# Kernel optimization log

Measured on AMD Instinct MI355X. Metric: run time of the kernel, lower is better.

The kernel has to match this reference:

```python
import jax, jax.numpy as jnp
import numpy as np

DIM = 1024
NUM_HEADS = 16
HEAD_DIM = DIM // NUM_HEADS
B, N = 4, 2048


def _rope_sin_cos(seq_len, head_dim, dtype=jnp.float32):
    inv_freq = 1.0 / (10000.0 ** (jnp.arange(0, head_dim, 2, dtype=jnp.float32) / head_dim))
    t = jnp.arange(seq_len, dtype=jnp.float32)
    freqs = jnp.einsum('i,j->ij', t, inv_freq)          # [N, head_dim/2]
    emb = jnp.concatenate([freqs, freqs], axis=-1)      # [N, head_dim]
    return jnp.sin(emb).astype(dtype), jnp.cos(emb).astype(dtype)


def _rotate_half(x):
    x1, x2 = jnp.split(x, 2, axis=-1)
    return jnp.concatenate([-x2, x1], axis=-1)


def setup_inputs() -> dict:
    key = jax.random.key(0)
    k1, k2, k3, k4, k5 = jax.random.split(key, 5)
    scale = 0.02
    return {
        'x': jax.random.normal(k1, (B, N, DIM), dtype=jnp.float32),
        'W_qkv': jax.random.normal(k2, (DIM, 3 * DIM), dtype=jnp.float32) * scale,
        'b_qkv': jax.random.normal(k3, (3 * DIM,), dtype=jnp.float32) * scale,
        'W_proj': jax.random.normal(k4, (DIM, DIM), dtype=jnp.float32) * scale,
        'b_proj': jax.random.normal(k5, (DIM,), dtype=jnp.float32) * scale,
    }


def reference(x, W_qkv, b_qkv, W_proj, b_proj):
    Bsz, Nlen, C = x.shape
    H, Dh = NUM_HEADS, HEAD_DIM
    qkv = x @ W_qkv + b_qkv                              # [B, N, 3C]
    q, k, v = jnp.split(qkv, 3, axis=-1)
    # [B, H, N, Dh]
    q = q.reshape(Bsz, Nlen, H, Dh).transpose(0, 2, 1, 3)
    k = k.reshape(Bsz, Nlen, H, Dh).transpose(0, 2, 1, 3)
    v = v.reshape(Bsz, Nlen, H, Dh).transpose(0, 2, 1, 3)
    sin, cos = _rope_sin_cos(Nlen, Dh, x.dtype)          # [N, Dh] each, broadcast
    q = q * cos + _rotate_half(q) * sin
    k = k * cos + _rotate_half(k) * sin
    scale = 1.0 / jnp.sqrt(jnp.asarray(Dh, x.dtype))
    scores = jnp.einsum('bhqd,bhkd->bhqk', q, k) * scale  # [B, H, N, N]
    attn = jax.nn.softmax(scores, axis=-1)
    out = jnp.einsum('bhqk,bhkd->bhqd', attn, v)          # [B, H, N, Dh]
    out = out.transpose(0, 2, 1, 3).reshape(Bsz, Nlen, C)
    return out @ W_proj + b_proj
```

## Files before the change

kernel.cpp:

```cpp
#include <hip/hip_runtime.h>
#include <hip/hip_bf16.h>
#include <math.h>

#define BSZ 4
#define NSEQ 2048
#define CDIM 1024
#define NH 16
#define DH 64
#define KC 64
#define KMAX_STRIDE 32

typedef _Float16 half8_t __attribute__((ext_vector_type(8)));
typedef _Float16 half4_t __attribute__((ext_vector_type(4)));
typedef float floatx4 __attribute__((ext_vector_type(4)));

#define GLOBAL_AS(p) ((const __attribute__((address_space(1))) void*)(p))
#define LDS_AS(p)    ((__attribute__((address_space(3))) void*)(p))

__global__ __launch_bounds__(256) void cast_x_kernel(
    const float* __restrict__ src, _Float16* __restrict__ dst) {
  const size_t i = ((size_t)blockIdx.x * 256 + threadIdx.x) * 8;
  float4 a = *(const float4*)(src + i);
  float4 b = *(const float4*)(src + i + 4);
  half8_t h;
  h[0] = (_Float16)a.x; h[1] = (_Float16)a.y; h[2] = (_Float16)a.z; h[3] = (_Float16)a.w;
  h[4] = (_Float16)b.x; h[5] = (_Float16)b.y; h[6] = (_Float16)b.z; h[7] = (_Float16)b.w;
  *(half8_t*)(dst + i) = h;
}

__global__ __launch_bounds__(256) void transpose_cast_kernel(
    const float* __restrict__ src, _Float16* __restrict__ dst, int R, int C) {
  __shared__ float Ls[64][65];
  const int t = threadIdx.x;
  const int r0 = blockIdx.y * 64, c0 = blockIdx.x * 64;
  {
    const int lr = t >> 2, lcg = (t & 3) * 16;
    const float* s = src + (size_t)(r0 + lr) * C + c0 + lcg;
#pragma unroll
    for (int u = 0; u < 4; ++u)
      *(float4*)&Ls[lr][lcg + 4 * u] = *(const float4*)(s + 4 * u);
  }
  __syncthreads();
  const int c = t >> 2, rg = (t & 3) * 16;
  half8_t h0, h1;
#pragma unroll
  for (int u = 0; u < 8; ++u) h0[u] = (_Float16)Ls[rg + u][c];
#pragma unroll
  for (int u = 0; u < 8; ++u) h1[u] = (_Float16)Ls[rg + 8 + u][c];
  _Float16* d = dst + (size_t)(c0 + c) * R + r0 + rg;
  *(half8_t*)d = h0;
  *(half8_t*)(d + 8) = h1;
}

__global__ __launch_bounds__(256) void qkv_gemm_kernel(
    const _Float16* __restrict__ xh, const _Float16* __restrict__ Wt,
    const float* __restrict__ bias, _Float16* __restrict__ Qh,
    _Float16* __restrict__ Kh, _Float16* __restrict__ Vh) {
  __shared__ _Float16 As[128 * 64];
  __shared__ _Float16 Bs[128 * 64];
  const int tid = threadIdx.x;
  const int lane = tid & 63, w = tid >> 6;
  const int m = lane & 15, quad = lane >> 4;
  const int wr = (w >> 1) * 64, wc = (w & 1) * 64;
  const int m0 = blockIdx.y * 128;
  const int N0 = blockIdx.x * 128;
  const int sr = lane >> 3, sc = (lane & 7) * 8;

  floatx4 acc[4][4];
#pragma unroll
  for (int i = 0; i < 4; ++i)
#pragma unroll
    for (int j = 0; j < 4; ++j) acc[i][j] = (floatx4){0.f, 0.f, 0.f, 0.f};

  for (int k0 = 0; k0 < CDIM; k0 += 64) {
    __syncthreads();
#pragma unroll
    for (int i = 0; i < 4; ++i) {
      const int row = (w * 4 + i) * 8 + sr;
      __builtin_amdgcn_global_load_lds(
          GLOBAL_AS(xh + (size_t)(m0 + row) * CDIM + k0 + sc),
          LDS_AS(As + (w * 4 + i) * 512), 16, 0, 0);
      __builtin_amdgcn_global_load_lds(
          GLOBAL_AS(Wt + (size_t)(N0 + row) * CDIM + k0 + sc),
          LDS_AS(Bs + (w * 4 + i) * 512), 16, 0, 0);
    }
    __syncthreads();
#pragma unroll
    for (int ks = 0; ks < 2; ++ks) {
      half8_t af[4], bf[4];
#pragma unroll
      for (int mt = 0; mt < 4; ++mt)
        af[mt] = *(half8_t*)(As + (wr + mt * 16 + m) * 64 + ks * 32 + quad * 8);
#pragma unroll
      for (int nt = 0; nt < 4; ++nt)
        bf[nt] = *(half8_t*)(Bs + (wc + nt * 16 + m) * 64 + ks * 32 + quad * 8);
#pragma unroll
      for (int mt = 0; mt < 4; ++mt)
#pragma unroll
        for (int nt = 0; nt < 4; ++nt)
          acc[mt][nt] = __builtin_amdgcn_mfma_f32_16x16x32_f16(
              af[mt], bf[nt], acc[mt][nt], 0, 0, 0);
    }
  }

  const int F0 = N0 + wc;
  const int which = F0 >> 10;
  const int head = (F0 & 1023) >> 6;
  float bv[4];
#pragma unroll
  for (int nt = 0; nt < 4; ++nt) bv[nt] = bias[F0 + nt * 16 + m];

  if (which == 2) {
#pragma unroll
    for (int mt = 0; mt < 4; ++mt)
#pragma unroll
      for (int reg = 0; reg < 4; ++reg) {
        const int gm = m0 + wr + mt * 16 + 4 * quad + reg;
        const int b = gm >> 11, n = gm & 2047;
        const size_t vbase = ((size_t)(b * NH + head) * DH) * NSEQ + n;
#pragma unroll
        for (int nt = 0; nt < 4; ++nt)
          Vh[vbase + (size_t)(nt * 16 + m) * NSEQ] =
              (_Float16)(acc[mt][nt][reg] + bv[nt]);
      }
  } else {
    _Float16* dst = which ? Kh : Qh;
    const float qs = which ? 1.0f : 0.125f * 1.4426950408889634f;
    const float invfA = expf(-9.210340371976184f * ((float)m * (1.0f / 32.0f)));
    const float invfB = expf(-9.210340371976184f * ((float)(16 + m) * (1.0f / 32.0f)));
#pragma unroll
    for (int mt = 0; mt < 4; ++mt)
#pragma unroll
      for (int reg = 0; reg < 4; ++reg) {
        const int gm = m0 + wr + mt * 16 + 4 * quad + reg;
        const int b = gm >> 11, n = gm & 2047;
        float sA, cA, sB, cB;
        sincosf((float)n * invfA, &sA, &cA);
        sincosf((float)n * invfB, &sB, &cB);
        const size_t obase = ((size_t)(b * NH + head) * NSEQ + n) * DH;
#pragma unroll
        for (int nt = 0; nt < 4; ++nt) {
          const float val = acc[mt][nt][reg] + bv[nt];
          const float rot = (nt < 2) ? -(acc[mt][nt + 2][reg] + bv[nt + 2])
                                     :  (acc[mt][nt - 2][reg] + bv[nt - 2]);
          const float sv = (nt & 1) ? sB : sA;
          const float cv = (nt & 1) ? cB : cA;
          dst[obase + nt * 16 + m] = (_Float16)((val * cv + rot * sv) * qs);
        }
      }
  }
}

__global__ __launch_bounds__(64) void kmax_init_kernel(unsigned* kmaxu) {
  for (int i = threadIdx.x; i < 64 * KMAX_STRIDE; i += 64) kmaxu[i] = 0u;
}

__global__ __launch_bounds__(256) void qk_norms_kernel(
    const _Float16* __restrict__ Qh, const _Float16* __restrict__ Kh,
    float* __restrict__ qn, unsigned* __restrict__ kmaxu) {
  __shared__ float wmax[4];
  const int tid = threadIdx.x;
  const size_t row = (size_t)blockIdx.x * 32 + (tid >> 3);
  const int c = (tid & 7) * 8;
  half8_t q8 = *(const half8_t*)(Qh + row * DH + c);
  half8_t k8 = *(const half8_t*)(Kh + row * DH + c);
  float qs = 0.f, ks = 0.f;
#pragma unroll
  for (int u = 0; u < 8; ++u) {
    const float qv = (float)q8[u], kv = (float)k8[u];
    qs += qv * qv; ks += kv * kv;
  }
  qs += __shfl_xor(qs, 1, 64); ks += __shfl_xor(ks, 1, 64);
  qs += __shfl_xor(qs, 2, 64); ks += __shfl_xor(ks, 2, 64);
  qs += __shfl_xor(qs, 4, 64); ks += __shfl_xor(ks, 4, 64);
  if ((tid & 7) == 0) qn[row] = sqrtf(qs);
  ks = fmaxf(ks, __shfl_xor(ks, 8, 64));
  ks = fmaxf(ks, __shfl_xor(ks, 16, 64));
  ks = fmaxf(ks, __shfl_xor(ks, 32, 64));
  if ((tid & 63) == 0) wmax[tid >> 6] = ks;
  __syncthreads();
  if (tid == 0) {
    const float mx = fmaxf(fmaxf(wmax[0], wmax[1]), fmaxf(wmax[2], wmax[3]));
    atomicMax(&kmaxu[(row >> 11) * KMAX_STRIDE], __float_as_uint(sqrtf(mx)));
  }
}

__global__ __launch_bounds__(256) void attn_kernel(
    const _Float16* __restrict__ Qh, const _Float16* __restrict__ Kh,
    const _Float16* __restrict__ Vh, const float* __restrict__ qn,
    const unsigned* __restrict__ kmaxu, _Float16* __restrict__ AO) {
  __shared__ char smem[36864];
  _Float16* Ks = (_Float16*)smem;
  _Float16* Vt = (_Float16*)(smem + 9216);
  _Float16* Ps = (_Float16*)(smem + 18432);
  float* Os = (float*)smem;

  const int tid = threadIdx.x;
  const int lane = tid & 63;
  const int w = tid >> 6;
  const int m = lane & 15;
  const int quad = lane >> 4;
  const int bh = blockIdx.y;
  const int q0 = blockIdx.x * 128;

  const _Float16* Qb = Qh + (size_t)bh * NSEQ * DH;
  const _Float16* Kb = Kh + (size_t)bh * NSEQ * DH;
  const _Float16* Vb = Vh + (size_t)bh * DH * NSEQ;

  const int rA = q0 + w * 32 + m;
  const int rB = rA + 16;
  half8_t qfA0 = *(const half8_t*)(Qb + (size_t)rA * DH + quad * 8);
  half8_t qfA1 = *(const half8_t*)(Qb + (size_t)rA * DH + 32 + quad * 8);
  half8_t qfB0 = *(const half8_t*)(Qb + (size_t)rB * DH + quad * 8);
  half8_t qfB1 = *(const half8_t*)(Qb + (size_t)rB * DH + 32 + quad * 8);

  const float kmx = __uint_as_float(kmaxu[bh * KMAX_STRIDE]);
  const float mA = qn[(size_t)bh * NSEQ + rA] * kmx;
  const float mB = qn[(size_t)bh * NSEQ + rB] * kmx;

  float lA = 0.f, lB = 0.f;
  floatx4 OA[4], OB[4];
#pragma unroll
  for (int nb = 0; nb < 4; ++nb) {
    OA[nb] = (floatx4){0.f, 0.f, 0.f, 0.f};
    OB[nb] = (floatx4){0.f, 0.f, 0.f, 0.f};
  }

  _Float16* PwA = Ps + w * 2304 + m * 72;
  _Float16* PwB = PwA + 16 * 72;

  for (int ck = 0; ck < NSEQ / KC; ++ck) {
    const int k0 = ck * KC;
    __syncthreads();
    {
      const _Float16* Kc = Kb + (size_t)k0 * DH;
      const _Float16* Vc = Vb + k0;
      int g = tid;
      int key = g >> 3, dg = g & 7;
      *(half8_t*)(Ks + key * 72 + dg * 8) = *(const half8_t*)(Kc + key * 64 + dg * 8);
      *(half8_t*)(Vt + key * 72 + dg * 8) = *(const half8_t*)(Vc + (size_t)key * NSEQ + dg * 8);
      g = tid + 256;
      key = g >> 3; dg = g & 7;
      *(half8_t*)(Ks + key * 72 + dg * 8) = *(const half8_t*)(Kc + key * 64 + dg * 8);
      *(half8_t*)(Vt + key * 72 + dg * 8) = *(const half8_t*)(Vc + (size_t)key * NSEQ + dg * 8);
    }
    __syncthreads();

    floatx4 stA[4], stB[4];
#pragma unroll
    for (int kt = 0; kt < 4; ++kt) {
      half8_t kf0 = *(half8_t*)(Ks + (kt * 16 + m) * 72 + quad * 8);
      half8_t kf1 = *(half8_t*)(Ks + (kt * 16 + m) * 72 + 32 + quad * 8);
      floatx4 a = (floatx4){0.f, 0.f, 0.f, 0.f};
      a = __builtin_amdgcn_mfma_f32_16x16x32_f16(kf0, qfA0, a, 0, 0, 0);
      a = __builtin_amdgcn_mfma_f32_16x16x32_f16(kf1, qfA1, a, 0, 0, 0);
      stA[kt] = a;
      floatx4 b = (floatx4){0.f, 0.f, 0.f, 0.f};
      b = __builtin_amdgcn_mfma_f32_16x16x32_f16(kf0, qfB0, b, 0, 0, 0);
      b = __builtin_amdgcn_mfma_f32_16x16x32_f16(kf1, qfB1, b, 0, 0, 0);
      stB[kt] = b;
    }

#pragma unroll
    for (int kt = 0; kt < 4; ++kt) {
      half4_t phA, phB;
#pragma unroll
      for (int r = 0; r < 4; ++r) {
        const float pA = __builtin_exp2f(stA[kt][r] - mA);
        const float pB = __builtin_exp2f(stB[kt][r] - mB);
        lA += pA; lB += pB;
        phA[r] = (_Float16)pA; phB[r] = (_Float16)pB;
      }
      *(half4_t*)(PwA + kt * 16 + quad * 4) = phA;
      *(half4_t*)(PwB + kt * 16 + quad * 4) = phB;
    }

#pragma unroll
    for (int c = 0; c < 2; ++c) {
      half8_t pfA = *(half8_t*)(PwA + c * 32 + quad * 8);
      half8_t pfB = *(half8_t*)(PwB + c * 32 + quad * 8);
#pragma unroll
      for (int nb = 0; nb < 4; ++nb) {
        half8_t vf = *(half8_t*)(Vt + (nb * 16 + m) * 72 + c * 32 + quad * 8);
        OA[nb] = __builtin_amdgcn_mfma_f32_16x16x32_f16(pfA, vf, OA[nb], 0, 0, 0);
        OB[nb] = __builtin_amdgcn_mfma_f32_16x16x32_f16(pfB, vf, OB[nb], 0, 0, 0);
      }
    }
  }

  lA += __shfl_xor(lA, 16, 64); lA += __shfl_xor(lA, 32, 64);
  lB += __shfl_xor(lB, 16, 64); lB += __shfl_xor(lB, 32, 64);
  float lA4[4], lB4[4];
#pragma unroll
  for (int r = 0; r < 4; ++r) {
    lA4[r] = __shfl(lA, 4 * quad + r, 64);
    lB4[r] = __shfl(lB, 4 * quad + r, 64);
  }
  __syncthreads();
#pragma unroll
  for (int nb = 0; nb < 4; ++nb) {
#pragma unroll
    for (int r = 0; r < 4; ++r) {
      Os[(w * 32 + 4 * quad + r) * 68 + nb * 16 + m] = OA[nb][r] * (1.0f / lA4[r]);
      Os[(w * 32 + 16 + 4 * quad + r) * 68 + nb * 16 + m] = OB[nb][r] * (1.0f / lB4[r]);
    }
  }
  __syncthreads();
  const int ql = tid >> 1, dg = (tid & 1) * 32;
  const int b = bh >> 4, h = bh & 15;
  _Float16* dst = AO + ((size_t)(b * NSEQ + q0 + ql)) * CDIM + h * DH + dg;
#pragma unroll
  for (int u = 0; u < 4; ++u) {
    half8_t o;
#pragma unroll
    for (int v = 0; v < 8; ++v) o[v] = (_Float16)Os[ql * 68 + dg + u * 8 + v];
    *(half8_t*)(dst + u * 8) = o;
  }
}

__global__ __launch_bounds__(256) void proj_gemm_kernel(
    const _Float16* __restrict__ Ah, const _Float16* __restrict__ Wt,
    const float* __restrict__ bias, float* __restrict__ out) {
  __shared__ _Float16 As[128 * 64];
  __shared__ _Float16 Bs[128 * 64];
  const int tid = threadIdx.x;
  const int lane = tid & 63, w = tid >> 6;
  const int m = lane & 15, quad = lane >> 4;
  const int wr = (w >> 1) * 64, wc = (w & 1) * 64;
  const int m0 = blockIdx.y * 128;
  const int N0 = blockIdx.x * 128;
  const int sr = lane >> 3, sc = (lane & 7) * 8;

  floatx4 acc[4][4];
#pragma unroll
  for (int i = 0; i < 4; ++i)
#pragma unroll
    for (int j = 0; j < 4; ++j) acc[i][j] = (floatx4){0.f, 0.f, 0.f, 0.f};

  for (int k0 = 0; k0 < CDIM; k0 += 64) {
    __syncthreads();
#pragma unroll
    for (int i = 0; i < 4; ++i) {
      const int row = (w * 4 + i) * 8 + sr;
      __builtin_amdgcn_global_load_lds(
          GLOBAL_AS(Ah + (size_t)(m0 + row) * CDIM + k0 + sc),
          LDS_AS(As + (w * 4 + i) * 512), 16, 0, 0);
      __builtin_amdgcn_global_load_lds(
          GLOBAL_AS(Wt + (size_t)(N0 + row) * CDIM + k0 + sc),
          LDS_AS(Bs + (w * 4 + i) * 512), 16, 0, 0);
    }
    __syncthreads();
#pragma unroll
    for (int ks = 0; ks < 2; ++ks) {
      half8_t af[4], bf[4];
#pragma unroll
      for (int mt = 0; mt < 4; ++mt)
        af[mt] = *(half8_t*)(As + (wr + mt * 16 + m) * 64 + ks * 32 + quad * 8);
#pragma unroll
      for (int nt = 0; nt < 4; ++nt)
        bf[nt] = *(half8_t*)(Bs + (wc + nt * 16 + m) * 64 + ks * 32 + quad * 8);
#pragma unroll
      for (int mt = 0; mt < 4; ++mt)
#pragma unroll
        for (int nt = 0; nt < 4; ++nt)
          acc[mt][nt] = __builtin_amdgcn_mfma_f32_16x16x32_f16(
              af[mt], bf[nt], acc[mt][nt], 0, 0, 0);
    }
  }

  const int F0 = N0 + wc;
  float bv[4];
#pragma unroll
  for (int nt = 0; nt < 4; ++nt) bv[nt] = bias[F0 + nt * 16 + m];
#pragma unroll
  for (int mt = 0; mt < 4; ++mt)
#pragma unroll
    for (int reg = 0; reg < 4; ++reg) {
      const int gm = m0 + wr + mt * 16 + 4 * quad + reg;
#pragma unroll
      for (int nt = 0; nt < 4; ++nt)
        out[(size_t)gm * CDIM + F0 + nt * 16 + m] = acc[mt][nt][reg] + bv[nt];
    }
}

extern "C" void kernel_launch(void* const* d_in, const int* in_sizes, int n_in,
                              void* d_out, int out_size, void* d_ws, size_t ws_size,
                              hipStream_t stream) {
  const float* x     = (const float*)d_in[0];
  const float* Wqkv  = (const float*)d_in[1];
  const float* bqkv  = (const float*)d_in[2];
  const float* Wproj = (const float*)d_in[3];
  const float* bproj = (const float*)d_in[4];
  float* out = (float*)d_out;

  const size_t per = (size_t)BSZ * NH * NSEQ * DH;
  _Float16* xh  = (_Float16*)d_ws;
  _Float16* Wt  = xh + per;
  _Float16* Wpt = Wt + (size_t)3072 * 1024;
  _Float16* Qh  = Wpt + (size_t)1024 * 1024;
  _Float16* Kh  = Qh + per;
  _Float16* Vh  = Kh + per;
  _Float16* AOh = Vh + per;
  float*    qnp = (float*)(AOh + per);
  unsigned* kmx = (unsigned*)(qnp + (size_t)64 * NSEQ);

  cast_x_kernel<<<4096, 256, 0, stream>>>(x, xh);
  transpose_cast_kernel<<<dim3(48, 16), 256, 0, stream>>>(Wqkv, Wt, 1024, 3072);
  transpose_cast_kernel<<<dim3(16, 16), 256, 0, stream>>>(Wproj, Wpt, 1024, 1024);
  kmax_init_kernel<<<1, 64, 0, stream>>>(kmx);
  qkv_gemm_kernel<<<dim3(24, 64), 256, 0, stream>>>(xh, Wt, bqkv, Qh, Kh, Vh);
  qk_norms_kernel<<<4096, 256, 0, stream>>>(Qh, Kh, qnp, kmx);
  attn_kernel<<<dim3(16, 64), 256, 0, stream>>>(Qh, Kh, Vh, qnp, kmx, AOh);
  proj_gemm_kernel<<<dim3(8, 64), 256, 0, stream>>>(AOh, Wpt, bproj, out);
}
```

Baseline: 350.0 us.

## Keep softmax probabilities in registers and feed PV MFMA directly, halving LDS

Drops the LDS round trip for the P tile. Exponentials computed from the QK MFMA output are packed to fp16 and fed straight into 16x16x16 MFMAs against V, because the 16x16 accumulator layout matches the A-operand layout of that instruction. The row max subtraction is folded into the accumulator init, and row sums use packed fdot2 on the fp16 values. The epilogue is also split into two passes so shared memory shrinks to 18 KB, which may raise occupancy, at the cost of smaller-K MFMAs and extra barriers.

```diff
diff --git a/kernel.cpp b/kernel.cpp
--- a/kernel.cpp
+++ b/kernel.cpp
@@ -12,6 +12,8 @@
 
 typedef _Float16 half8_t __attribute__((ext_vector_type(8)));
 typedef _Float16 half4_t __attribute__((ext_vector_type(4)));
+typedef __fp16 pk2_t __attribute__((ext_vector_type(2)));
+typedef __fp16 pk4_t __attribute__((ext_vector_type(4)));
 typedef float floatx4 __attribute__((ext_vector_type(4)));
 
 #define GLOBAL_AS(p) ((const __attribute__((address_space(1))) void*)(p))
@@ -189,10 +191,9 @@
     const _Float16* __restrict__ Qh, const _Float16* __restrict__ Kh,
     const _Float16* __restrict__ Vh, const float* __restrict__ qn,
     const unsigned* __restrict__ kmaxu, _Float16* __restrict__ AO) {
-  __shared__ char smem[36864];
+  __shared__ char smem[18432];
   _Float16* Ks = (_Float16*)smem;
   _Float16* Vt = (_Float16*)(smem + 9216);
-  _Float16* Ps = (_Float16*)(smem + 18432);
   float* Os = (float*)smem;
 
   const int tid = threadIdx.x;
@@ -218,6 +219,16 @@
   const float mA = qn[(size_t)bh * NSEQ + rA] * kmx;
   const float mB = qn[(size_t)bh * NSEQ + rB] * kmx;
 
+  const int skey = tid >> 3, sdg = (tid & 7) * 8;
+  const _Float16* ksrc0 = Kb + (size_t)skey * DH + sdg;
+  const _Float16* ksrc1 = Kb + (size_t)(skey + 32) * DH + sdg;
+  const _Float16* vsrc0 = Vb + (size_t)skey * NSEQ + sdg;
+  const _Float16* vsrc1 = Vb + (size_t)(skey + 32) * NSEQ + sdg;
+  _Float16* kdst0 = Ks + skey * 72 + sdg;
+  _Float16* kdst1 = Ks + (skey + 32) * 72 + sdg;
+  _Float16* vdst0 = Vt + skey * 72 + sdg;
+  _Float16* vdst1 = Vt + (skey + 32) * 72 + sdg;
+
   float lA = 0.f, lB = 0.f;
   floatx4 OA[4], OB[4];
 #pragma unroll
@@ -225,65 +236,53 @@
     OA[nb] = (floatx4){0.f, 0.f, 0.f, 0.f};
     OB[nb] = (floatx4){0.f, 0.f, 0.f, 0.f};
   }
-
-  _Float16* PwA = Ps + w * 2304 + m * 72;
-  _Float16* PwB = PwA + 16 * 72;
+  const pk2_t one2 = {(__fp16)1.f, (__fp16)1.f};
 
   for (int ck = 0; ck < NSEQ / KC; ++ck) {
-    const int k0 = ck * KC;
-    __syncthreads();
-    {
-      const _Float16* Kc = Kb + (size_t)k0 * DH;
-      const _Float16* Vc = Vb + k0;
-      int g = tid;
-      int key = g >> 3, dg = g & 7;
-      *(half8_t*)(Ks + key * 72 + dg * 8) = *(const half8_t*)(Kc + key * 64 + dg * 8);
-      *(half8_t*)(Vt + key * 72 + dg * 8) = *(const half8_t*)(Vc + (size_t)key * NSEQ + dg * 8);
-      g = tid + 256;
-      key = g >> 3; dg = g & 7;
-      *(half8_t*)(Ks + key * 72 + dg * 8) = *(const half8_t*)(Kc + key * 64 + dg * 8);
-      *(half8_t*)(Vt + key * 72 + dg * 8) = *(const half8_t*)(Vc + (size_t)key * NSEQ + dg * 8);
-    }
-    __syncthreads();
-
-    floatx4 stA[4], stB[4];
+    __syncthreads();
+    *(half8_t*)kdst0 = *(const half8_t*)ksrc0;  ksrc0 += KC * DH;
+    *(half8_t*)kdst1 = *(const half8_t*)ksrc1;  ksrc1 += KC * DH;
+    *(half8_t*)vdst0 = *(const half8_t*)vsrc0;  vsrc0 += KC;
+    *(half8_t*)vdst1 = *(const half8_t*)vsrc1;  vsrc1 += KC;
+    __syncthreads();
+
 #pragma unroll
     for (int kt = 0; kt < 4; ++kt) {
       half8_t kf0 = *(half8_t*)(Ks + (kt * 16 + m) * 72 + quad * 8);
       half8_t kf1 = *(half8_t*)(Ks + (kt * 16 + m) * 72 + 32 + quad * 8);
-      floatx4 a = (floatx4){0.f, 0.f, 0.f, 0.f};
+      floatx4 a = (floatx4){-mA, -mA, -mA, -mA};
       a = __builtin_amdgcn_mfma_f32_16x16x32_f16(kf0, qfA0, a, 0, 0, 0);
       a = __builtin_amdgcn_mfma_f32_16x16x32_f16(kf1, qfA1, a, 0, 0, 0);
-      stA[kt] = a;
-      floatx4 b = (floatx4){0.f, 0.f, 0.f, 0.f};
+      floatx4 b = (floatx4){-mB, -mB, -mB, -mB};
       b = __builtin_amdgcn_mfma_f32_16x16x32_f16(kf0, qfB0, b, 0, 0, 0);
       b = __builtin_amdgcn_mfma_f32_16x16x32_f16(kf1, qfB1, b, 0, 0, 0);
-      stB[kt] = b;
-    }
-
-#pragma unroll
-    for (int kt = 0; kt < 4; ++kt) {
-      half4_t phA, phB;
-#pragma unroll
-      for (int r = 0; r < 4; ++r) {
-        const float pA = __builtin_exp2f(stA[kt][r] - mA);
-        const float pB = __builtin_exp2f(stB[kt][r] - mB);
-        lA += pA; lB += pB;
-        phA[r] = (_Float16)pA; phB[r] = (_Float16)pB;
-      }
-      *(half4_t*)(PwA + kt * 16 + quad * 4) = phA;
-      *(half4_t*)(PwB + kt * 16 + quad * 4) = phB;
-    }
-
-#pragma unroll
-    for (int c = 0; c < 2; ++c) {
-      half8_t pfA = *(half8_t*)(PwA + c * 32 + quad * 8);
-      half8_t pfB = *(half8_t*)(PwB + c * 32 + quad * 8);
+
+      const float pA0 = __builtin_exp2f(a[0]);
+      const float pA1 = __builtin_exp2f(a[1]);
+      const float pA2 = __builtin_exp2f(a[2]);
+      const float pA3 = __builtin_exp2f(a[3]);
+      const float pB0 = __builtin_exp2f(b[0]);
+      const float pB1 = __builtin_exp2f(b[1]);
+      const float pB2 = __builtin_exp2f(b[2]);
+      const float pB3 = __builtin_exp2f(b[3]);
+      pk2_t a01 = __builtin_amdgcn_cvt_pkrtz(pA0, pA1);
+      pk2_t a23 = __builtin_amdgcn_cvt_pkrtz(pA2, pA3);
+      pk2_t b01 = __builtin_amdgcn_cvt_pkrtz(pB0, pB1);
+      pk2_t b23 = __builtin_amdgcn_cvt_pkrtz(pB2, pB3);
+      lA = __builtin_amdgcn_fdot2(a01, one2, lA, false);
+      lA = __builtin_amdgcn_fdot2(a23, one2, lA, false);
+      lB = __builtin_amdgcn_fdot2(b01, one2, lB, false);
+      lB = __builtin_amdgcn_fdot2(b23, one2, lB, false);
+      half4_t phA = __builtin_bit_cast(
+          half4_t, (pk4_t)__builtin_shufflevector(a01, a23, 0, 1, 2, 3));
+      half4_t phB = __builtin_bit_cast(
+          half4_t, (pk4_t)__builtin_shufflevector(b01, b23, 0, 1, 2, 3));
+
 #pragma unroll
       for (int nb = 0; nb < 4; ++nb) {
-        half8_t vf = *(half8_t*)(Vt + (nb * 16 + m) * 72 + c * 32 + quad * 8);
-        OA[nb] = __builtin_amdgcn_mfma_f32_16x16x32_f16(pfA, vf, OA[nb], 0, 0, 0);
-        OB[nb] = __builtin_amdgcn_mfma_f32_16x16x32_f16(pfB, vf, OB[nb], 0, 0, 0);
+        half4_t vf = *(half4_t*)(Vt + (nb * 16 + m) * 72 + kt * 16 + quad * 4);
+        OA[nb] = __builtin_amdgcn_mfma_f32_16x16x16f16(phA, vf, OA[nb], 0, 0, 0);
+        OB[nb] = __builtin_amdgcn_mfma_f32_16x16x16f16(phB, vf, OB[nb], 0, 0, 0);
       }
     }
   }
@@ -296,25 +295,41 @@
     lA4[r] = __shfl(lA, 4 * quad + r, 64);
     lB4[r] = __shfl(lB, 4 * quad + r, 64);
   }
-  __syncthreads();
-#pragma unroll
-  for (int nb = 0; nb < 4; ++nb) {
-#pragma unroll
-    for (int r = 0; r < 4; ++r) {
-      Os[(w * 32 + 4 * quad + r) * 68 + nb * 16 + m] = OA[nb][r] * (1.0f / lA4[r]);
-      Os[(w * 32 + 16 + 4 * quad + r) * 68 + nb * 16 + m] = OB[nb][r] * (1.0f / lB4[r]);
-    }
-  }
-  __syncthreads();
-  const int ql = tid >> 1, dg = (tid & 1) * 32;
+
   const int b = bh >> 4, h = bh & 15;
-  _Float16* dst = AO + ((size_t)(b * NSEQ + q0 + ql)) * CDIM + h * DH + dg;
-#pragma unroll
-  for (int u = 0; u < 4; ++u) {
+  const int ql = tid >> 2, dgo = (tid & 3) * 16;
+  const int gq = q0 + (ql >> 4) * 32 + (ql & 15);
+  _Float16* dstA = AO + ((size_t)(b * NSEQ + gq)) * CDIM + h * DH + dgo;
+
+  __syncthreads();
+#pragma unroll
+  for (int nb = 0; nb < 4; ++nb)
+#pragma unroll
+    for (int r = 0; r < 4; ++r)
+      Os[(w * 16 + 4 * quad + r) * 68 + nb * 16 + m] = OA[nb][r] * (1.0f / lA4[r]);
+  __syncthreads();
+#pragma unroll
+  for (int u = 0; u < 2; ++u) {
     half8_t o;
 #pragma unroll
-    for (int v = 0; v < 8; ++v) o[v] = (_Float16)Os[ql * 68 + dg + u * 8 + v];
-    *(half8_t*)(dst + u * 8) = o;
+    for (int v = 0; v < 8; ++v) o[v] = (_Float16)Os[ql * 68 + dgo + u * 8 + v];
+    *(half8_t*)(dstA + u * 8) = o;
+  }
+
+  __syncthreads();
+#pragma unroll
+  for (int nb = 0; nb < 4; ++nb)
+#pragma unroll
+    for (int r = 0; r < 4; ++r)
+      Os[(w * 16 + 4 * quad + r) * 68 + nb * 16 + m] = OB[nb][r] * (1.0f / lB4[r]);
+  __syncthreads();
+  _Float16* dstB = dstA + (size_t)16 * CDIM;
+#pragma unroll
+  for (int u = 0; u < 2; ++u) {
+    half8_t o;
+#pragma unroll
+    for (int v = 0; v < 8; ++v) o[v] = (_Float16)Os[ql * 68 + dgo + u * 8 + v];
+    *(half8_t*)(dstB + u * 8) = o;
   }
 }
 
```

Result: no change. 351.0 us (+0.3%).
